# Kernel tuning notes

Hardware: AMD Instinct MI355X
Metric: run time of the kernel (lower is better)

Reference implementation:

```python
import jax, jax.numpy as jnp
import numpy as np

# Rs_hidden = [(16,0),(16,1)] -> 16 scalar irreps (dim 1) then 16 vector irreps (dim 3)
B, N, M = 4, 80, 16
CH = M + 3 * M  # 64 channels
RADII = jnp.linspace(0.0, 1.0, 3)
GAMMA = 1.0 / (0.5 ** 2)  # gaussian rbf width = radii spacing
EPS = 1e-6

_lc = np.zeros((3, 3, 3), np.float32)
for i, j, k in [(0, 1, 2), (1, 2, 0), (2, 0, 1)]:
    _lc[i, j, k] = 1.0
    _lc[i, k, j] = -1.0
LC = jnp.asarray(_lc)  # Levi-Civita


def _si(t, w0, w1):
    """SelfInteraction: per-l mixing of multiplicities. t: [B, mi0 + 3*mi1, ...]."""
    mi0, mi1 = w0.shape[1], w1.shape[1]
    s = t[:, :mi0]
    v = t[:, mi0:].reshape(t.shape[0], mi1, 3, *t.shape[2:])
    os = jnp.einsum('om,nm...->no...', w0, s)
    ov = jnp.einsum('om,nmi...->noi...', w1, v)
    ov = ov.reshape(ov.shape[0], ov.shape[1] * 3, *ov.shape[3:])
    return jnp.concatenate([os, ov], axis=1)


def _norm_act(t, act):
    """NormActivation: scalar irreps -> act(x); vector irreps -> x * act(||x||)/||x||. Channel axis 1."""
    s = act(t[:, :M])
    v = t[:, M:].reshape(t.shape[0], M, 3, *t.shape[2:])
    n = jnp.sqrt(jnp.sum(v * v, axis=2, keepdims=True) + EPS)
    v = (v * act(n) / n).reshape(t.shape[0], 3 * M, *t.shape[2:])
    return jnp.concatenate([s, v], axis=1)


def _gate_mul(gate, target):
    """gate_normwise_multiply: multiply each irrep block of target by the L2 norm of the
    corresponding gate block (norm over the irrep components, channel axis 1)."""
    gs = jnp.abs(gate[:, :M])
    gv = gate[:, M:].reshape(gate.shape[0], M, 3, *gate.shape[2:])
    gn = jnp.sqrt(jnp.sum(gv * gv, axis=2) + EPS)
    factor = jnp.concatenate([gs, jnp.repeat(gn, 3, axis=1)], axis=1)
    return factor * target


def _interleave(a_t, b_t):
    """Interleave per-(m,l) blocks: [a_l0, b_l0, a_l1, b_l1] -> Rs_hidden_double layout."""
    return jnp.concatenate([a_t[:, :M], b_t[:, :M], a_t[:, M:], b_t[:, M:]], axis=1)


def _kernel(h_nei_diff, w_k00, w_k10, w_k01, w_k11):
    """SE3 point kernel for l in {0,1}, J<=2. Returns K[n,b,a,d,c] with d,c in irrep layout."""
    rad = jnp.sqrt(jnp.sum(h_nei_diff ** 2, axis=-1) + EPS)      # [B,N,N]
    nh = h_nei_diff / rad[..., None]                              # unit vectors
    rbf = jnp.exp(-GAMMA * (rad[..., None] - RADII) ** 2)        # [B,N,N,3]
    K00 = jnp.einsum('uvk,...k->...uv', w_k00, rbf)              # [B,N,N,M,M]
    K10 = jnp.einsum('uvk,...k,...i->...uiv', w_k10, rbf, nh).reshape(B, N, N, 3 * M, M)
    K01 = jnp.einsum('uvk,...k,...j->...uvj', w_k01, rbf, nh).reshape(B, N, N, M, 3 * M)
    RJ = jnp.einsum('juvk,...k->j...uv', w_k11, rbf)             # [3,B,N,N,M,M]
    eye = jnp.eye(3, dtype=rbf.dtype)
    cross = jnp.einsum('ijk,...k->...ij', LC, nh)                # J=1 basis
    outer = nh[..., :, None] * nh[..., None, :] - eye / 3.0      # J=2 basis
    base = (RJ[0][..., None, None] * eye
            + RJ[1][..., None, None] * cross[..., None, None, :, :]
            + RJ[2][..., None, None] * outer[..., None, None, :, :])  # [B,N,N,u,v,i,j]
    K11 = jnp.transpose(base, (0, 1, 2, 3, 5, 4, 6)).reshape(B, N, N, 3 * M, 3 * M)
    top = jnp.concatenate([K00, K01], axis=-1)
    bot = jnp.concatenate([K10, K11], axis=-1)
    return jnp.concatenate([top, bot], axis=-2)                  # [B,N,N,CH,CH]


def setup_inputs() -> dict:
    key = jax.random.key(0)
    ks = jax.random.split(key, 16)
    sc = 0.1
    d = {
        'x': jax.random.normal(ks[0], (B, CH, N), jnp.float32),
        'h_nei': jax.random.normal(ks[1], (B, CH, N), jnp.float32),
        'h_nei_diff': jax.random.normal(ks[2], (B, N, N, 3), jnp.float32),
        'mask': jax.random.uniform(ks[3], (B, N, N), jnp.float32),
        'w_k00': jax.random.normal(ks[4], (M, M, 3), jnp.float32) * sc,
        'w_k10': jax.random.normal(ks[5], (M, M, 3), jnp.float32) * sc,
        'w_k01': jax.random.normal(ks[6], (M, M, 3), jnp.float32) * sc,
        'w_k11': jax.random.normal(ks[7], (3, M, M, 3), jnp.float32) * sc,
        'si_z_w0': jax.random.normal(ks[8], (M, 2 * M), jnp.float32) * sc,
        'si_z_w1': jax.random.normal(ks[9], (M, 2 * M), jnp.float32) * sc,
        'si_r1_w0': jax.random.normal(ks[10], (M, M), jnp.float32) * sc,
        'si_r1_w1': jax.random.normal(ks[11], (M, M), jnp.float32) * sc,
        'si_r2_w0': jax.random.normal(ks[12], (M, M), jnp.float32) * sc,
        'si_r2_w1': jax.random.normal(ks[13], (M, M), jnp.float32) * sc,
        'si_ph_w0': jax.random.normal(ks[14], (M, 2 * M), jnp.float32) * sc,
        'si_ph_w1': jax.random.normal(ks[15], (M, 2 * M), jnp.float32) * sc,
    }
    return d


def reference(x, h_nei, h_nei_diff, mask, w_k00, w_k10, w_k01, w_k11,
              si_z_w0, si_z_w1, si_r1_w0, si_r1_w1, si_r2_w0, si_r2_w1,
              si_ph_w0, si_ph_w1):
    Kmat = _kernel(h_nei_diff, w_k00, w_k10, w_k01, w_k11)
    # masked neighbor conv: h_conv[n,d,b,a] = sum_c h_nei[n,c,a] K[n,b,a,d,c] mask[n,b,a]
    h_conv = jnp.einsum('nca,nbadc,nba->ndba', h_nei, Kmat, mask)
    sum_h = h_conv.sum(axis=-1)                                   # [B,CH,N]
    z = _norm_act(_si(_interleave(x, sum_h), si_z_w0, si_z_w1), jax.nn.sigmoid)
    r1 = _si(x, si_r1_w0, si_r1_w1)                               # [B,CH,N]
    r2 = _si(h_conv.reshape(B, CH, N * N), si_r2_w0, si_r2_w1).reshape(B, CH, N, N)
    r = _norm_act(r1[:, :, None, :] + r2, jax.nn.sigmoid)         # [B,CH,N,N]
    gated = _gate_mul(r, h_conv)
    sum_g = gated.sum(axis=-1)                                    # [B,CH,N]
    pre_h = _norm_act(_si(_interleave(x, sum_g), si_ph_w0, si_ph_w1), jnp.tanh)
    new_h = sum_h + _gate_mul(z, pre_h + sum_h)
    return new_h
```

## Files before the change

### kernel.cpp

```cpp
#include <hip/hip_runtime.h>
#include <math.h>

#define Bq 4
#define Nq 80
#define CHq 64
#define GAMMAq 4.0f
#define EPSq 1e-6f
#define PCWL 100
#define NQUAD 24


__global__ __launch_bounds__(192) void se3_precomp(
    const float* __restrict__ h_nei,
    const float* __restrict__ x,
    const float* __restrict__ w00,
    const float* __restrict__ w10,
    const float* __restrict__ w01,
    const float* __restrict__ w11,
    const float* __restrict__ wr10,
    const float* __restrict__ wr11,
    const float* __restrict__ wr20,
    const float* __restrict__ wr21,
    float* __restrict__ pc)
{
    const int L   = blockIdx.x & 7;
    const int idx = blockIdx.x >> 3;
    const int n   = L >> 1;
    const int a   = (L & 1) * 40 + idx;
    const int na  = n * Nq + a;
    const int tid = threadIdx.x;

    __shared__ float hsh[64];
    __shared__ float xsh[64];
    __shared__ float psh[2][42][16];
    __shared__ float r1sh[2][4][16];
    __shared__ float pout[16][PCWL];

    if (tid < 64)       hsh[tid]      = h_nei[(size_t)n * CHq * Nq + tid * Nq + a];
    else if (tid < 128) xsh[tid - 64] = x    [(size_t)n * CHq * Nq + (tid - 64) * Nq + a];
    __syncthreads();

    if (tid < 128) {
        const int u    = tid & 15;
        const int q    = tid >> 4;
        const int half = q & 1;
        const int kk   = q >> 1;
        const int v0   = half * 8;

        if (kk < 3) {
            const int k = kk;
            float a00 = 0.f, a10 = 0.f;
            float c[3] = {0.f,0.f,0.f}, p0[3] = {0.f,0.f,0.f};
            float p1[3] = {0.f,0.f,0.f}, p2[3] = {0.f,0.f,0.f};
#pragma unroll
            for (int i = 0; i < 8; ++i) {
                const int v = v0 + i;
                const float s = hsh[v];
                a00 += w00[(u * 16 + v) * 3 + k] * s;
                a10 += w10[(u * 16 + v) * 3 + k] * s;
                const float w01v = w01[(u * 16 + v) * 3 + k];
                const float w110 = w11[((0 * 16 + u) * 16 + v) * 3 + k];
                const float w111 = w11[((1 * 16 + u) * 16 + v) * 3 + k];
                const float w112 = w11[((2 * 16 + u) * 16 + v) * 3 + k];
#pragma unroll
                for (int j = 0; j < 3; ++j) {
                    const float Vj = hsh[16 + v * 3 + j];
                    c[j]  += w01v * Vj;
                    p0[j] += w110 * Vj;
                    p1[j] += w111 * Vj;
                    p2[j] += w112 * Vj;
                }
            }
            psh[half][0 + k][u] = a00;
            psh[half][3 + k][u] = a10;
#pragma unroll
            for (int j = 0; j < 3; ++j) {
                psh[half][6  + k * 3 + j][u] = c[j];
                psh[half][15 + k * 3 + j][u] = p0[j];
                psh[half][24 + k * 3 + j][u] = p1[j];
                psh[half][33 + k * 3 + j][u] = p2[j];
            }
        } else {
            float r1s = 0.f, r1v[3] = {0.f, 0.f, 0.f};
#pragma unroll
            for (int i = 0; i < 8; ++i) {
                const int v = v0 + i;
                r1s += wr10[u * 16 + v] * xsh[v];
                const float wv = wr11[u * 16 + v];
#pragma unroll
                for (int j = 0; j < 3; ++j) r1v[j] += wv * xsh[16 + v * 3 + j];
            }
            r1sh[half][0][u] = r1s;
#pragma unroll
            for (int j = 0; j < 3; ++j) r1sh[half][1 + j][u] = r1v[j];
        }
    }
    __syncthreads();

    if (tid < 96) {
        const int u  = tid & 15;
        const int kk = tid >> 4;
#pragma unroll
        for (int c = kk * 7; c < kk * 7 + 7; ++c)
            pout[u][c] = psh[0][c][u] + psh[1][c][u];
        if (kk == 0) {
#pragma unroll
            for (int j = 0; j < 4; ++j)
                pout[u][42 + j] = r1sh[0][j][u] + r1sh[1][j][u];
            pout[u][46] = 0.f; pout[u][47] = 0.f;
#pragma unroll
            for (int j = 90; j < 96; ++j) pout[u][j] = 0.f;
        }
    }
    __syncthreads();

    if (tid < 96) {
        const int u  = tid & 15;
        const int kk = tid >> 4;
#pragma unroll
        for (int c = kk * 7; c < kk * 7 + 7; ++c) {
            const bool scalarType = (c < 3) || (c >= 6 && c < 15);
            const float* W = scalarType ? wr20 : wr21;
            float acc = 0.f;
#pragma unroll
            for (int v = 0; v < 16; ++v) acc += W[u * 16 + v] * pout[v][c];
            pout[u][48 + c] = acc;
        }
    }
    __syncthreads();

    {
        float4* dst = reinterpret_cast<float4*>(pc) + (size_t)na * (NQUAD * 16);
#pragma unroll
        for (int i = 0; i < 2; ++i) {
            const int qi = tid + i * 192;
            const int c4 = qi >> 4;
            const int u  = qi & 15;
            dst[c4 * 16 + u] = make_float4(pout[u][c4 * 4 + 0], pout[u][c4 * 4 + 1],
                                           pout[u][c4 * 4 + 2], pout[u][c4 * 4 + 3]);
        }
    }
}

__global__ __launch_bounds__(256) void se3_main(
    const float* __restrict__ x,
    const float* __restrict__ hdiff,
    const float* __restrict__ mask,
    const float* __restrict__ wz0,
    const float* __restrict__ wz1,
    const float* __restrict__ wp0,
    const float* __restrict__ wp1,
    const float* __restrict__ pc,
    float* __restrict__ out)
{
    const int L     = blockIdx.x & 7;
    const int idx   = blockIdx.x >> 3;
    const int n     = L >> 1;
    const int bnode = (L & 1) * 40 + idx;
    const int tid   = threadIdx.x;
    const int g     = tid >> 4;
    const int u     = tid & 15;

    __shared__ float wsh[4][512];
    __shared__ float redW[4][8][16];
    __shared__ float sumHs[64], sumGs[64];

#pragma unroll
    for (int i = 0; i < 2; ++i) {
        const int widx = tid + i * 256;
        wsh[0][widx] = wz0[widx];
        wsh[1][widx] = wz1[widx];
        wsh[2][widx] = wp0[widx];
        wsh[3][widx] = wp1[widx];
    }

    float shs = 0.f, shv0 = 0.f, shv1 = 0.f, shv2 = 0.f;
    float sgs = 0.f, sgv0 = 0.f, sgv1 = 0.f, sgv2 = 0.f;

    const float* drow = hdiff + (size_t)(n * Nq + bnode) * Nq * 3;
    const float* mrow = mask  + (size_t)(n * Nq + bnode) * Nq;
    const float third = 1.0f / 3.0f;

    for (int it = 0; it < 5; ++it) {
        const int a = it * 16 + g;

        const float d0 = drow[a * 3 + 0], d1 = drow[a * 3 + 1], d2 = drow[a * 3 + 2];
        const float m  = mrow[a];

        const float rad = sqrtf(d0 * d0 + d1 * d1 + d2 * d2 + EPSq);
        const float inv = 1.0f / rad;
        const float nh0 = d0 * inv, nh1 = d1 * inv, nh2 = d2 * inv;
        float rb[3];
        rb[0] = __expf(-GAMMAq * rad * rad);
        { float t1 = rad - 0.5f; rb[1] = __expf(-GAMMAq * t1 * t1); }
        { float t2 = rad - 1.0f; rb[2] = __expf(-GAMMAq * t2 * t2); }

        const float4* p4 = reinterpret_cast<const float4*>(pc)
                         + (size_t)(n * Nq + a) * (NQUAD * 16) + u;

        float pa[48];
#pragma unroll
        for (int i = 0; i < 12; ++i)
            *reinterpret_cast<float4*>(&pa[i * 4]) = p4[i * 16];
        float pb[44];
#pragma unroll
        for (int i = 0; i < 11; ++i)
            *reinterpret_cast<float4*>(&pb[i * 4]) = p4[(12 + i) * 16];

        float as_ = 0.f, a10 = 0.f;
        float c01[3] = {0.f,0.f,0.f}, p0[3] = {0.f,0.f,0.f};
        float p1[3] = {0.f,0.f,0.f}, p2[3] = {0.f,0.f,0.f};
        float bs_ = 0.f, b10 = 0.f;
        float bc01[3] = {0.f,0.f,0.f}, bp0[3] = {0.f,0.f,0.f};
        float bp1[3] = {0.f,0.f,0.f}, bp2[3] = {0.f,0.f,0.f};
#pragma unroll
        for (int k = 0; k < 3; ++k) {
            const float r = rb[k];
            as_ += r * pa[0 + k];
            a10 += r * pa[3 + k];
            bs_ += r * pb[0 + k];
            b10 += r * pb[3 + k];
#pragma unroll
            for (int j = 0; j < 3; ++j) {
                c01[j]  += r * pa[6  + k * 3 + j];
                p0[j]   += r * pa[15 + k * 3 + j];
                p1[j]   += r * pa[24 + k * 3 + j];
                p2[j]   += r * pa[33 + k * 3 + j];
                bc01[j] += r * pb[6  + k * 3 + j];
                bp0[j]  += r * pb[15 + k * 3 + j];
                bp1[j]  += r * pb[24 + k * 3 + j];
                bp2[j]  += r * pb[33 + k * 3 + j];
            }
        }

        const float hcs = m * (as_ + c01[0] * nh0 + c01[1] * nh1 + c01[2] * nh2);
        const float cr0 = p1[1] * nh2 - p1[2] * nh1;
        const float cr1 = p1[2] * nh0 - p1[0] * nh2;
        const float cr2 = p1[0] * nh1 - p1[1] * nh0;
        const float pd  = p2[0] * nh0 + p2[1] * nh1 + p2[2] * nh2;
        const float hv0 = m * (nh0 * a10 + p0[0] + cr0 + nh0 * pd - p2[0] * third);
        const float hv1 = m * (nh1 * a10 + p0[1] + cr1 + nh1 * pd - p2[1] * third);
        const float hv2 = m * (nh2 * a10 + p0[2] + cr2 + nh2 * pd - p2[2] * third);

        const float r2s = m * (bs_ + bc01[0] * nh0 + bc01[1] * nh1 + bc01[2] * nh2);
        const float br0 = bp1[1] * nh2 - bp1[2] * nh1;
        const float br1 = bp1[2] * nh0 - bp1[0] * nh2;
        const float br2 = bp1[0] * nh1 - bp1[1] * nh0;
        const float bpd = bp2[0] * nh0 + bp2[1] * nh1 + bp2[2] * nh2;
        const float r2v0 = m * (nh0 * b10 + bp0[0] + br0 + nh0 * bpd - bp2[0] * third);
        const float r2v1 = m * (nh1 * b10 + bp0[1] + br1 + nh1 * bpd - bp2[1] * third);
        const float r2v2 = m * (nh2 * b10 + bp0[2] + br2 + nh2 * bpd - bp2[2] * third);

        const float r1s  = pa[42];
        const float r1v0 = pa[43], r1v1 = pa[44], r1v2 = pa[45];

        const float rs  = 1.0f / (1.0f + __expf(-(r1s + r2s)));
        const float wv0 = r1v0 + r2v0, wv1 = r1v1 + r2v1, wv2 = r1v2 + r2v2;
        const float nn  = sqrtf(wv0 * wv0 + wv1 * wv1 + wv2 * wv2 + EPSq);
        const float sc  = (1.0f / (1.0f + __expf(-nn))) / nn;
        const float rv0 = wv0 * sc, rv1 = wv1 * sc, rv2 = wv2 * sc;
        const float fs  = fabsf(rs);
        const float fv  = sqrtf(rv0 * rv0 + rv1 * rv1 + rv2 * rv2 + EPSq);

        shs += hcs;        shv0 += hv0;      shv1 += hv1;      shv2 += hv2;
        sgs += fs * hcs;   sgv0 += fv * hv0; sgv1 += fv * hv1; sgv2 += fv * hv2;
    }

    float vals[8] = {shs, shv0, shv1, shv2, sgs, sgv0, sgv1, sgv2};
#pragma unroll
    for (int q = 0; q < 8; ++q) {
        vals[q] += __shfl_xor(vals[q], 16, 64);
        vals[q] += __shfl_xor(vals[q], 32, 64);
    }
    const int wave = tid >> 6;
    if ((tid & 63) < 16) {
#pragma unroll
        for (int q = 0; q < 8; ++q) redW[wave][q][u] = vals[q];
    }
    __syncthreads();

    if (tid < 16) {
        float tacc[8];
#pragma unroll
        for (int q = 0; q < 8; ++q)
            tacc[q] = redW[0][q][tid] + redW[1][q][tid] + redW[2][q][tid] + redW[3][q][tid];
        sumHs[tid] = tacc[0];
        sumGs[tid] = tacc[4];
#pragma unroll
        for (int j = 0; j < 3; ++j) {
            sumHs[16 + tid * 3 + j] = tacc[1 + j];
            sumGs[16 + tid * 3 + j] = tacc[5 + j];
        }
    }
    __syncthreads();

    if (tid < 16) {
        const float* xb = x + (size_t)n * CHq * Nq + bnode;

        float zs_in = 0.f, ps_in = 0.f;
        float zv[3] = {0.f, 0.f, 0.f};
        float pv[3] = {0.f, 0.f, 0.f};
#pragma unroll
        for (int mm = 0; mm < 32; ++mm) {
            float Sh, Sg;
            if (mm < 16) { const float xv = xb[mm * Nq]; Sh = xv; Sg = xv; }
            else         { Sh = sumHs[mm - 16]; Sg = sumGs[mm - 16]; }
            zs_in += wsh[0][tid * 32 + mm] * Sh;
            ps_in += wsh[2][tid * 32 + mm] * Sg;
            const float wz = wsh[1][tid * 32 + mm];
            const float wp = wsh[3][tid * 32 + mm];
#pragma unroll
            for (int j = 0; j < 3; ++j) {
                float Vh, Vg;
                if (mm < 16) { const float xv = xb[(16 + mm * 3 + j) * Nq]; Vh = xv; Vg = xv; }
                else { Vh = sumHs[16 + (mm - 16) * 3 + j]; Vg = sumGs[16 + (mm - 16) * 3 + j]; }
                zv[j] += wz * Vh;
                pv[j] += wp * Vg;
            }
        }

        const float zs  = 1.0f / (1.0f + __expf(-zs_in));
        const float zn  = sqrtf(zv[0] * zv[0] + zv[1] * zv[1] + zv[2] * zv[2] + EPSq);
        const float zsc = (1.0f / (1.0f + __expf(-zn))) / zn;
        const float zv0 = zv[0] * zsc, zv1 = zv[1] * zsc, zv2 = zv[2] * zsc;
        const float phs = tanhf(ps_in);
        const float pn  = sqrtf(pv[0] * pv[0] + pv[1] * pv[1] + pv[2] * pv[2] + EPSq);
        const float psc = tanhf(pn) / pn;
        const float pv0 = pv[0] * psc, pv1 = pv[1] * psc, pv2 = pv[2] * psc;
        const float gfs = fabsf(zs);
        const float gfv = sqrtf(zv0 * zv0 + zv1 * zv1 + zv2 * zv2 + EPSq);

        float* ob = out + (size_t)n * CHq * Nq + bnode;
        const float sh_s = sumHs[tid];
        ob[tid * Nq] = sh_s + gfs * (phs + sh_s);
#pragma unroll
        for (int j = 0; j < 3; ++j) {
            const float shv = sumHs[16 + tid * 3 + j];
            const float pvj = (j == 0) ? pv0 : ((j == 1) ? pv1 : pv2);
            ob[(16 + tid * 3 + j) * Nq] = shv + gfv * (pvj + shv);
        }
    }
}

extern "C" void kernel_launch(void* const* d_in, const int* in_sizes, int n_in,
                              void* d_out, int out_size, void* d_ws, size_t ws_size,
                              hipStream_t stream) {
    const float* x      = (const float*)d_in[0];
    const float* h_nei  = (const float*)d_in[1];
    const float* hdiff  = (const float*)d_in[2];
    const float* mask   = (const float*)d_in[3];
    const float* w00    = (const float*)d_in[4];
    const float* w10    = (const float*)d_in[5];
    const float* w01    = (const float*)d_in[6];
    const float* w11    = (const float*)d_in[7];
    const float* wz0    = (const float*)d_in[8];
    const float* wz1    = (const float*)d_in[9];
    const float* wr10   = (const float*)d_in[10];
    const float* wr11   = (const float*)d_in[11];
    const float* wr20   = (const float*)d_in[12];
    const float* wr21   = (const float*)d_in[13];
    const float* wp0    = (const float*)d_in[14];
    const float* wp1    = (const float*)d_in[15];
    float* out = (float*)d_out;
    float* pc  = (float*)d_ws;

    se3_precomp<<<Bq * Nq, 192, 0, stream>>>(
        h_nei, x, w00, w10, w01, w11, wr10, wr11, wr20, wr21, pc);
    se3_main<<<Bq * Nq, 256, 0, stream>>>(
        x, hdiff, mask, wz0, wz1, wp0, wp1, pc, out);
}
```

Measured before the change: 24.86 us.

## Stage precomp weights in padded LDS and double-buffer main-kernel precomputed loads

In the precompute kernel, kernel weights are first copied into padded shared memory so the inner reduction reads LDS without bank conflicts instead of doing strided global loads. In the main kernel, hdiff and mask values for all five iterations are loaded up front, and the per-neighbour precomputed coefficients are register double-buffered so the next iteration's loads overlap the current math. Launch bounds are set to one block per SM to give room for the extra ~92 registers, at the cost of occupancy and possible spills.

Measured after the change: 24.03 us (median of 3 runs). 3.3% less time.

```diff
diff --git a/kernel.cpp b/kernel.cpp
--- a/kernel.cpp
+++ b/kernel.cpp
@@ -32,12 +32,31 @@
 
     __shared__ float hsh[64];
     __shared__ float xsh[64];
+    __shared__ float w00s[784], w10s[784], w01s[784];
+    __shared__ float w11s[3][784];
+    __shared__ float wr10s[272], wr11s[272];
     __shared__ float psh[2][42][16];
     __shared__ float r1sh[2][4][16];
     __shared__ float pout[16][PCWL];
 
     if (tid < 64)       hsh[tid]      = h_nei[(size_t)n * CHq * Nq + tid * Nq + a];
     else if (tid < 128) xsh[tid - 64] = x    [(size_t)n * CHq * Nq + (tid - 64) * Nq + a];
+
+    for (int e = tid; e < 768; e += 192) {
+        const int u = e / 48, r = e - u * 48;
+        const int d = u * 49 + r;
+        w00s[d]    = w00[e];
+        w10s[d]    = w10[e];
+        w01s[d]    = w01[e];
+        w11s[0][d] = w11[e];
+        w11s[1][d] = w11[768 + e];
+        w11s[2][d] = w11[1536 + e];
+    }
+    for (int e = tid; e < 256; e += 192) {
+        const int u = e >> 4, v = e & 15;
+        wr10s[u * 17 + v] = wr10[e];
+        wr11s[u * 17 + v] = wr11[e];
+    }
     __syncthreads();
 
     if (tid < 128) {
@@ -54,14 +73,15 @@
             float p1[3] = {0.f,0.f,0.f}, p2[3] = {0.f,0.f,0.f};
 #pragma unroll
             for (int i = 0; i < 8; ++i) {
-                const int v = v0 + i;
+                const int v  = v0 + i;
+                const int wi = u * 49 + v * 3 + k;
                 const float s = hsh[v];
-                a00 += w00[(u * 16 + v) * 3 + k] * s;
-                a10 += w10[(u * 16 + v) * 3 + k] * s;
-                const float w01v = w01[(u * 16 + v) * 3 + k];
-                const float w110 = w11[((0 * 16 + u) * 16 + v) * 3 + k];
-                const float w111 = w11[((1 * 16 + u) * 16 + v) * 3 + k];
-                const float w112 = w11[((2 * 16 + u) * 16 + v) * 3 + k];
+                a00 += w00s[wi] * s;
+                a10 += w10s[wi] * s;
+                const float w01v = w01s[wi];
+                const float w110 = w11s[0][wi];
+                const float w111 = w11s[1][wi];
+                const float w112 = w11s[2][wi];
 #pragma unroll
                 for (int j = 0; j < 3; ++j) {
                     const float Vj = hsh[16 + v * 3 + j];
@@ -85,8 +105,8 @@
 #pragma unroll
             for (int i = 0; i < 8; ++i) {
                 const int v = v0 + i;
-                r1s += wr10[u * 16 + v] * xsh[v];
-                const float wv = wr11[u * 16 + v];
+                r1s += wr10s[u * 17 + v] * xsh[v];
+                const float wv = wr11s[u * 17 + v];
 #pragma unroll
                 for (int j = 0; j < 3; ++j) r1v[j] += wv * xsh[16 + v * 3 + j];
             }
@@ -142,7 +162,7 @@
     }
 }
 
-__global__ __launch_bounds__(256) void se3_main(
+__global__ __launch_bounds__(256, 1) void se3_main(
     const float* __restrict__ x,
     const float* __restrict__ hdiff,
     const float* __restrict__ mask,
@@ -174,18 +194,55 @@
         wsh[3][widx] = wp1[widx];
     }
 
-    float shs = 0.f, shv0 = 0.f, shv1 = 0.f, shv2 = 0.f;
-    float sgs = 0.f, sgv0 = 0.f, sgv1 = 0.f, sgv2 = 0.f;
-
     const float* drow = hdiff + (size_t)(n * Nq + bnode) * Nq * 3;
     const float* mrow = mask  + (size_t)(n * Nq + bnode) * Nq;
     const float third = 1.0f / 3.0f;
 
+    float dg[5][3], mg[5];
+#pragma unroll
     for (int it = 0; it < 5; ++it) {
         const int a = it * 16 + g;
-
-        const float d0 = drow[a * 3 + 0], d1 = drow[a * 3 + 1], d2 = drow[a * 3 + 2];
-        const float m  = mrow[a];
+        dg[it][0] = drow[a * 3 + 0];
+        dg[it][1] = drow[a * 3 + 1];
+        dg[it][2] = drow[a * 3 + 2];
+        mg[it]    = mrow[a];
+    }
+
+    const float4* pcbase = reinterpret_cast<const float4*>(pc)
+                         + (size_t)(n * Nq) * (NQUAD * 16) + u;
+
+    float shs = 0.f, shv0 = 0.f, shv1 = 0.f, shv2 = 0.f;
+    float sgs = 0.f, sgv0 = 0.f, sgv1 = 0.f, sgv2 = 0.f;
+
+    float pa[2][48], pb[2][44];
+
+    {
+        const float4* p4 = pcbase + (size_t)g * (NQUAD * 16);
+#pragma unroll
+        for (int i = 0; i < 12; ++i)
+            *reinterpret_cast<float4*>(&pa[0][i * 4]) = p4[i * 16];
+#pragma unroll
+        for (int i = 0; i < 11; ++i)
+            *reinterpret_cast<float4*>(&pb[0][i * 4]) = p4[(12 + i) * 16];
+    }
+
+#pragma unroll
+    for (int it = 0; it < 5; ++it) {
+        const int cur = it & 1, nxt = cur ^ 1;
+
+        if (it < 4) {
+            const int a2 = (it + 1) * 16 + g;
+            const float4* p4 = pcbase + (size_t)a2 * (NQUAD * 16);
+#pragma unroll
+            for (int i = 0; i < 12; ++i)
+                *reinterpret_cast<float4*>(&pa[nxt][i * 4]) = p4[i * 16];
+#pragma unroll
+            for (int i = 0; i < 11; ++i)
+                *reinterpret_cast<float4*>(&pb[nxt][i * 4]) = p4[(12 + i) * 16];
+        }
+
+        const float d0 = dg[it][0], d1 = dg[it][1], d2 = dg[it][2];
+        const float m  = mg[it];
 
         const float rad = sqrtf(d0 * d0 + d1 * d1 + d2 * d2 + EPSq);
         const float inv = 1.0f / rad;
@@ -195,18 +252,6 @@
         { float t1 = rad - 0.5f; rb[1] = __expf(-GAMMAq * t1 * t1); }
         { float t2 = rad - 1.0f; rb[2] = __expf(-GAMMAq * t2 * t2); }
 
-        const float4* p4 = reinterpret_cast<const float4*>(pc)
-                         + (size_t)(n * Nq + a) * (NQUAD * 16) + u;
-
-        float pa[48];
-#pragma unroll
-        for (int i = 0; i < 12; ++i)
-            *reinterpret_cast<float4*>(&pa[i * 4]) = p4[i * 16];
-        float pb[44];
-#pragma unroll
-        for (int i = 0; i < 11; ++i)
-            *reinterpret_cast<float4*>(&pb[i * 4]) = p4[(12 + i) * 16];
-
         float as_ = 0.f, a10 = 0.f;
         float c01[3] = {0.f,0.f,0.f}, p0[3] = {0.f,0.f,0.f};
         float p1[3] = {0.f,0.f,0.f}, p2[3] = {0.f,0.f,0.f};
@@ -216,20 +261,20 @@
 #pragma unroll
         for (int k = 0; k < 3; ++k) {
             const float r = rb[k];
-            as_ += r * pa[0 + k];
-            a10 += r * pa[3 + k];
-            bs_ += r * pb[0 + k];
-            b10 += r * pb[3 + k];
+            as_ += r * pa[cur][0 + k];
+            a10 += r * pa[cur][3 + k];
+            bs_ += r * pb[cur][0 + k];
+            b10 += r * pb[cur][3 + k];
 #pragma unroll
             for (int j = 0; j < 3; ++j) {
-                c01[j]  += r * pa[6  + k * 3 + j];
-                p0[j]   += r * pa[15 + k * 3 + j];
-                p1[j]   += r * pa[24 + k * 3 + j];
-                p2[j]   += r * pa[33 + k * 3 + j];
-                bc01[j] += r * pb[6  + k * 3 + j];
-                bp0[j]  += r * pb[15 + k * 3 + j];
-                bp1[j]  += r * pb[24 + k * 3 + j];
-                bp2[j]  += r * pb[33 + k * 3 + j];
+                c01[j]  += r * pa[cur][6  + k * 3 + j];
+                p0[j]   += r * pa[cur][15 + k * 3 + j];
+                p1[j]   += r * pa[cur][24 + k * 3 + j];
+                p2[j]   += r * pa[cur][33 + k * 3 + j];
+                bc01[j] += r * pb[cur][6  + k * 3 + j];
+                bp0[j]  += r * pb[cur][15 + k * 3 + j];
+                bp1[j]  += r * pb[cur][24 + k * 3 + j];
+                bp2[j]  += r * pb[cur][33 + k * 3 + j];
             }
         }
 
@@ -251,8 +296,8 @@
         const float r2v1 = m * (nh1 * b10 + bp0[1] + br1 + nh1 * bpd - bp2[1] * third);
         const float r2v2 = m * (nh2 * b10 + bp0[2] + br2 + nh2 * bpd - bp2[2] * third);
 
-        const float r1s  = pa[42];
-        const float r1v0 = pa[43], r1v1 = pa[44], r1v2 = pa[45];
+        const float r1s  = pa[cur][42];
+        const float r1v0 = pa[cur][43], r1v1 = pa[cur][44], r1v2 = pa[cur][45];
 
         const float rs  = 1.0f / (1.0f + __expf(-(r1s + r2s)));
         const float wv0 = r1v0 + r2v0, wv1 = r1v1 + r2v1, wv2 = r1v2 + r2v2;
```
